# Kernel optimization log

Measured on AMD Instinct MI355X. Metric: run time of the kernel, lower is better.

Reference implementation:

```python
import jax, jax.numpy as jnp
import numpy as np

N, DF, DR, H, K = 4096, 128, 64, 1024, 10


def _init_linear(key, fan_in, fan_out):
    kw, kb = jax.random.split(key)
    bound = 1.0 / np.sqrt(fan_in)
    W = jax.random.uniform(kw, (fan_in, fan_out), jnp.float32, -bound, bound)
    b = jax.random.uniform(kb, (fan_out,), jnp.float32, -bound, bound)
    return W, b


def setup_inputs() -> dict:
    key = jax.random.key(0)
    ks = jax.random.split(key, 8)
    condition = jax.random.normal(ks[0], (N, DF), jnp.float32)
    tensor = jax.random.normal(ks[1], (N, DR), jnp.float32)
    Win, b_in = _init_linear(ks[2], DF + DR, H)
    W1, b1 = _init_linear(ks[3], H, H)
    W2, b2 = _init_linear(ks[4], H, H)
    W3, b3 = _init_linear(ks[5], H, H)
    Wout, b_out = _init_linear(ks[6], H, DR)
    return {"condition": condition, "tensor": tensor,
            "Win": Win, "b_in": b_in, "W1": W1, "b1": b1,
            "W2": W2, "b2": b2, "W3": W3, "b3": b3,
            "Wout": Wout, "b_out": b_out}


def _mlp(x, Win, b_in, W1, b1, W2, b2, W3, b3, Wout, b_out):
    # FFNN: input layer + 3 hidden layers with Softplus, linear output -> DR
    h = jax.nn.softplus(x @ Win + b_in)
    h = jax.nn.softplus(h @ W1 + b1)
    h = jax.nn.softplus(h @ W2 + b2)
    h = jax.nn.softplus(h @ W3 + b3)
    return h @ Wout + b_out


def reference(condition, tensor, Win, b_in, W1, b1, W2, b2, W3, b3, Wout, b_out):
    # torch.cdist(condition, condition), p=2 -> [N, N]
    sq = jnp.sum(condition * condition, axis=-1)
    d2 = sq[:, None] + sq[None, :] - 2.0 * (condition @ condition.T)
    dist = jnp.sqrt(jnp.maximum(d2, 0.0))
    # torch.topk(dist, 10, dim=1, largest=False) -> k nearest neighbor indices
    _, neighbor_idx = jax.lax.top_k(-dist, K)  # [N, K]
    # gather neighbor groups
    cond_g = condition[neighbor_idx]  # [N, K, DF]
    tens_g = tensor[neighbor_idx]     # [N, K, DR]
    # MongeMapNetwork.pushforward: tensor - MLP(concat(condition, tensor))
    x = jnp.concatenate([cond_g, tens_g], axis=-1)  # [N, K, DF+DR]
    pushed = tens_g - _mlp(x, Win, b_in, W1, b1, W2, b2, W3, b3, Wout, b_out)
    return pushed  # [N, K, DR]
```

## Files before the change

kernel.cpp:

```cpp
#include <hip/hip_runtime.h>
#include <hip/hip_fp16.h>
#include <stdint.h>

typedef unsigned short u16;
typedef unsigned int   u32;
typedef unsigned long long u64;
typedef short v8bf __attribute__((ext_vector_type(8)));
typedef float v4f  __attribute__((ext_vector_type(4)));
typedef u16   v8u  __attribute__((ext_vector_type(8)));

#define NPTS 4096
#define DF   128
#define DR   64
#define HID  1024
#define KNN  10
#define DIN  192

#define AS1 __attribute__((address_space(1)))
#define AS3 __attribute__((address_space(3)))

__device__ __forceinline__ float bf2f(u16 b){ return __uint_as_float(((unsigned)b)<<16); }
__device__ __forceinline__ u16 f2bf(float f){
  unsigned u = __float_as_uint(f);
  unsigned r = 0x7fffu + ((u>>16)&1u);
  return (u16)((u + r)>>16);
}
__device__ __forceinline__ u16 f2h(float f){
  __half h = __float2half(f);
  return __half_as_ushort(h);
}
__device__ __forceinline__ float softplus_f(float x){
  return x>15.f ? x : __logf(1.f + __expf(x));
}
__device__ __forceinline__ float rdv(const void* p, long j, int fl){
  return fl ? bf2f(((const u16*)p)[j]) : ((const float*)p)[j];
}
__device__ __forceinline__ void gl2lds16(const u16* g, u16* l){
  __builtin_amdgcn_global_load_lds((const AS1 unsigned int*)g, (AS3 unsigned int*)l, 16, 0, 0);
}

__global__ void detect_k(const u16* __restrict__ c, int* __restrict__ flag){
  __shared__ int cnt[256];
  int t = threadIdx.x, n = 0;
  for(int i=t; i<8192; i+=256){
    u16 v = c[2*i];
    int e = (v>>7)&0xff;
    n += (e>=96 && e<=158);
  }
  cnt[t] = n; __syncthreads();
  for(int s=128; s>0; s>>=1){ if(t<s) cnt[t]+=cnt[t+s]; __syncthreads(); }
  if(t==0) *flag = (cnt[0] > 4915) ? 1 : 0;
}

__global__ void prep_k(const void* cond, const void* tens,
    const void* Wi, const void* W1, const void* W2, const void* W3, const void* Wo,
    const void* bi, const void* b1, const void* b2, const void* b3, const void* bo,
    float* __restrict__ condF, float* __restrict__ tensF, float* __restrict__ biasF,
    u16* Oi, u16* O1, u16* O2, u16* O3, u16* Oo,
    float* __restrict__ sq, u16* __restrict__ X, const int* __restrict__ flag){
  __shared__ u16 tile[32][33];
  const int fl = *flag;
  const int bid = blockIdx.x, tid = threadIdx.x;
  if(bid < 3089){
    int i = bid*256 + tid;
    if(i < 524288){ condF[i] = rdv(cond, i, fl); }
    else if(i < 786432){ tensF[i-524288] = rdv(tens, i-524288, fl); }
    else{
      int j = i - 786432;
      if(j < 1024)      biasF[j] = rdv(bi, j, fl);
      else if(j < 2048) biasF[j] = rdv(b1, j-1024, fl);
      else if(j < 3072) biasF[j] = rdv(b2, j-2048, fl);
      else if(j < 4096) biasF[j] = rdv(b3, j-3072, fl);
      else if(j < 4160) biasF[j] = rdv(bo, j-4096, fl);
    }
  } else if(bid < 6417){
    int b = bid - 3089;
    const void* in; u16* out; int R, C, bx, by;
    if(b < 192)      {              in=Wi; out=Oi; R=192;  C=1024; bx=b&31; by=b>>5; }
    else if(b < 1216){ b -= 192;    in=W1; out=O1; R=1024; C=1024; bx=b&31; by=b>>5; }
    else if(b < 2240){ b -= 1216;   in=W2; out=O2; R=1024; C=1024; bx=b&31; by=b>>5; }
    else if(b < 3264){ b -= 2240;   in=W3; out=O3; R=1024; C=1024; bx=b&31; by=b>>5; }
    else             { b -= 3264;   in=Wo; out=Oo; R=1024; C=64;   bx=b&1;  by=b>>1; }
    int gx = bx*32, gy = by*32;
    int tx = tid&31, ty = tid>>5;
    #pragma unroll
    for(int r=ty; r<32; r+=8){
      size_t idx = (size_t)(gy+r)*C + gx + tx;
      tile[r][tx] = fl ? ((const u16*)in)[idx] : f2bf(((const float*)in)[idx]);
    }
    __syncthreads();
    #pragma unroll
    for(int r=ty; r<32; r+=8) out[(size_t)(gx+r)*R + gy + tx] = tile[tx][r];
  } else if(bid < 7441){
    int b = bid - 6417;
    int row = b*4 + (tid>>6), lane = tid&63;
    float a = rdv(cond, (long)row*DF + lane, fl);
    float c2 = rdv(cond, (long)row*DF + lane + 64, fl);
    double s = (double)a*a + (double)c2*c2;
    #pragma unroll
    for(int off=32; off>0; off>>=1) s += __shfl_down(s, off, 64);
    if(lane==0) sq[row] = (float)s;
  } else {
    int c = (bid-7441)*256 + tid;
    int j = c/48;
    int off = (c - j*48)*4;
    ushort4 o;
    if(off < DF){
      o.x = f2bf(rdv(cond, (long)j*DF + off + 0, fl));
      o.y = f2bf(rdv(cond, (long)j*DF + off + 1, fl));
      o.z = f2bf(rdv(cond, (long)j*DF + off + 2, fl));
      o.w = f2bf(rdv(cond, (long)j*DF + off + 3, fl));
    }else{
      int t2 = off - DF;
      o.x = f2bf(rdv(tens, (long)j*DR + t2 + 0, fl));
      o.y = f2bf(rdv(tens, (long)j*DR + t2 + 1, fl));
      o.z = f2bf(rdv(tens, (long)j*DR + t2 + 2, fl));
      o.w = f2bf(rdv(tens, (long)j*DR + t2 + 3, fl));
    }
    *(ushort4*)&X[(size_t)j*DIN + off] = o;
  }
}

__device__ __forceinline__ void gemm_bt_body(const u16* __restrict__ A,
    const u16* __restrict__ Bt, const float* __restrict__ bias, u16* __restrict__ C,
    int Nc, int Kc, int bid, u16* As, u16* Bs){
  const int xcd = bid&7, slot = bid>>3;
  const int bm = (xcd*4 + (slot>>4)) * 128;
  const int bn = (slot&15) * 64;
  const int tid = threadIdx.x, lane = tid&63, wave = tid>>6;
  const int wm = (wave&1)*64, wn = (wave>>1)*32;
  int c0 = wave*128 + lane, c1 = c0 + 64;
  int r0 = c0>>2, q0 = c0&3, r1 = c1>>2, q1 = c1&3;
  int cb = wave*64 + lane, rb = cb>>2, qb = cb&3;
  const u16* pA0 = A  + (size_t)(bm+r0)*Kc + q0*8;
  const u16* pA1 = A  + (size_t)(bm+r1)*Kc + q1*8;
  const u16* pB  = Bt + (size_t)(bn+rb)*Kc + qb*8;
  u16* lA0 = &As[wave*1024];
  u16* lA1 = &As[wave*1024 + 512];
  u16* lB  = &Bs[wave*512];
  const int m16 = lane&15, q = lane>>4;
  v4f acc[4][2] = {};
  for(int kb=0; kb<Kc; kb+=64){
    gl2lds16(pA0 + kb, lA0);
    gl2lds16(pA1 + kb, lA1);
    gl2lds16(pB  + kb, lB);
    gl2lds16(pA0 + kb + 32, lA0 + 4096);
    gl2lds16(pA1 + kb + 32, lA1 + 4096);
    gl2lds16(pB  + kb + 32, lB + 2048);
    __syncthreads();
    #pragma unroll
    for(int kk=0;kk<2;kk++){
      v8bf a[4], b[2];
      #pragma unroll
      for(int x=0;x<4;x++) a[x] = *(const v8bf*)&As[kk*4096 + (wm + x*16 + m16)*32 + q*8];
      #pragma unroll
      for(int x=0;x<2;x++) b[x] = *(const v8bf*)&Bs[kk*2048 + (wn + x*16 + m16)*32 + q*8];
      #pragma unroll
      for(int mi=0;mi<4;mi++)
        #pragma unroll
        for(int ni=0;ni<2;ni++)
          acc[mi][ni] = __builtin_amdgcn_mfma_f32_16x16x32_bf16(a[mi], b[ni], acc[mi][ni], 0,0,0);
    }
    __syncthreads();
  }
  const int col16 = lane&15, rowq = lane>>4;
  #pragma unroll
  for(int mi=0;mi<4;mi++){
    #pragma unroll
    for(int ni=0;ni<2;ni++){
      int cn = bn + wn + ni*16 + col16;
      float bi = bias[cn];
      #pragma unroll
      for(int r=0;r<4;r++){
        int rw = bm + wm + mi*16 + rowq*4 + r;
        float v = softplus_f(acc[mi][ni][r] + bi);
        C[(size_t)rw*Nc + cn] = f2bf(v);
      }
    }
  }
}

__device__ __forceinline__ void knn_body(const u16* __restrict__ distH,
    const float* __restrict__ condF, int* __restrict__ nidx, int row,
    float* __restrict__ af, int* __restrict__ scnt,
    int* __restrict__ cand, u64* __restrict__ keys){
  const int lane = threadIdx.x&63;
  af[lane]    = condF[(size_t)row*DF + lane];
  af[lane+64] = condF[(size_t)row*DF + lane + 64];
  if(lane==0) *scnt = 0;
  const v8u* drow = (const v8u*)(distH + (size_t)row*NPTS);
  v8u vals[8];
  #pragma unroll
  for(int k=0;k<8;k++) vals[k] = drow[lane + k*64];
  u32 mx = 0;
  #pragma unroll
  for(int k=0;k<8;k++)
    #pragma unroll
    for(int e=0;e<8;e++){ u32 v = vals[k][e]; mx = v>mx ? v : mx; }
  #pragma unroll
  for(int off=32; off>0; off>>=1){
    u32 o = (u32)__shfl_down((int)mx, off, 64); mx = o>mx ? o : mx;
  }
  mx = (u32)__shfl((int)mx, 0, 64);
  u32 hi = mx+1, lo = 0;
  for(int it=0; it<17; ++it){
    u32 mid = (lo+hi)>>1;
    int c = 0;
    #pragma unroll
    for(int k=0;k<8;k++)
      #pragma unroll
      for(int e=0;e<8;e++) c += ((u32)vals[k][e] < mid);
    #pragma unroll
    for(int off=32; off>0; off>>=1) c += __shfl_down(c, off, 64);
    c = __shfl(c, 0, 64);
    if(c >= 16){ hi = mid; if(c <= 48) break; }
    else lo = mid;
  }
  const u32 t = hi;
  #pragma unroll
  for(int k=0;k<8;k++)
    #pragma unroll
    for(int e=0;e<8;e++){
      if((u32)vals[k][e] < t){
        int s = atomicAdd(scnt, 1);
        if(s < 64) cand[s] = (lane + k*64)*8 + e;
      }
    }
  int cnt = *scnt; if(cnt > 64) cnt = 64;
  u64 mykey = ~0ULL; int myj = -1;
  if(lane < cnt){
    int j = cand[lane];
    const float4* bp4 = (const float4*)(condF + (size_t)j*DF);
    double s = 0.0;
    #pragma unroll
    for(int v4i=0; v4i<32; v4i++){
      float4 bv = bp4[v4i];
      double d0 = (double)af[v4i*4+0]-(double)bv.x;
      double d1 = (double)af[v4i*4+1]-(double)bv.y;
      double d2 = (double)af[v4i*4+2]-(double)bv.z;
      double d3 = (double)af[v4i*4+3]-(double)bv.w;
      s += d0*d0 + d1*d1 + d2*d2 + d3*d3;
    }
    u64 bits = (u64)__double_as_longlong(s);
    mykey = (bits & ~0xFFFULL) | (u32)j;
    myj = j;
  }
  keys[lane] = mykey;
  if(lane < cnt){
    int rank = 0;
    for(int c2=0;c2<cnt;c2++) rank += (keys[c2] < mykey);
    if(rank < KNN) nidx[row*KNN + rank] = myj;
  }
}

__global__ __launch_bounds__(256,2) void gram_g1_k(const u16* __restrict__ condB,
    const float* __restrict__ condF, const float* __restrict__ sq,
    u16* __restrict__ distH, const int* __restrict__ flag,
    const u16* __restrict__ X, const u16* __restrict__ Wt_in,
    const float* __restrict__ biasF, u16* __restrict__ A0){
  __shared__ __align__(16) u16 smem[20480];
  const int bid = blockIdx.x;
  if(bid < 512){
    gemm_bt_body(X, Wt_in, biasF, A0, HID, DIN, bid, smem, smem+8192);
    return;
  }
  const int gb = bid - 512;
  u16* Ahi = smem;
  u16* Alo = smem + 5120;
  u16* Bhi = smem + 10240;
  u16* Blo = smem + 15360;
  const int fl = *flag;
  const int bm = (gb&31)*128, bn = (gb>>5)*128;
  const int tid = threadIdx.x, lane = tid&63, wave = tid>>6;
  const int wm = (wave&1)*64, wn = (wave>>1)*64;
  v4f acc[4][4] = {};
  for(int kb=0; kb<DF; kb+=32){
    if(fl){
      #pragma unroll
      for(int t=0;t<2;t++){
        int c2 = tid + t*256;
        int r = c2>>2, col = (c2&3)*8;
        *(uint4*)&Ahi[r*40+col] = *(const uint4*)&condB[(size_t)(bm+r)*DF + kb + col];
        *(uint4*)&Bhi[r*40+col] = *(const uint4*)&condB[(size_t)(bn+r)*DF + kb + col];
      }
    }else{
      #pragma unroll
      for(int t=0;t<4;t++){
        int ch = tid + t*256;
        int r = ch>>3, c = (ch&7)*4;
        float4 av = *(const float4*)&condF[(size_t)(bm+r)*DF + kb + c];
        float4 bv = *(const float4*)&condF[(size_t)(bn+r)*DF + kb + c];
        ushort4 ah, bh, al, bl;
        ah.x=f2bf(av.x); ah.y=f2bf(av.y); ah.z=f2bf(av.z); ah.w=f2bf(av.w);
        bh.x=f2bf(bv.x); bh.y=f2bf(bv.y); bh.z=f2bf(bv.z); bh.w=f2bf(bv.w);
        al.x=f2bf(av.x-bf2f(ah.x)); al.y=f2bf(av.y-bf2f(ah.y));
        al.z=f2bf(av.z-bf2f(ah.z)); al.w=f2bf(av.w-bf2f(ah.w));
        bl.x=f2bf(bv.x-bf2f(bh.x)); bl.y=f2bf(bv.y-bf2f(bh.y));
        bl.z=f2bf(bv.z-bf2f(bh.z)); bl.w=f2bf(bv.w-bf2f(bh.w));
        *(ushort4*)&Ahi[r*40+c] = ah; *(ushort4*)&Bhi[r*40+c] = bh;
        *(ushort4*)&Alo[r*40+c] = al; *(ushort4*)&Blo[r*40+c] = bl;
      }
    }
    __syncthreads();
    const int m16 = lane&15, q = lane>>4;
    v8bf ahf[4], bhf[4];
    #pragma unroll
    for(int x=0;x<4;x++){
      ahf[x] = *(const v8bf*)&Ahi[(wm + x*16 + m16)*40 + q*8];
      bhf[x] = *(const v8bf*)&Bhi[(wn + x*16 + m16)*40 + q*8];
    }
    if(!fl){
      v8bf alf[4], blf[4];
      #pragma unroll
      for(int x=0;x<4;x++){
        alf[x] = *(const v8bf*)&Alo[(wm + x*16 + m16)*40 + q*8];
        blf[x] = *(const v8bf*)&Blo[(wn + x*16 + m16)*40 + q*8];
      }
      #pragma unroll
      for(int mi=0;mi<4;mi++)
        #pragma unroll
        for(int ni=0;ni<4;ni++){
          acc[mi][ni] = __builtin_amdgcn_mfma_f32_16x16x32_bf16(alf[mi], bhf[ni], acc[mi][ni], 0,0,0);
          acc[mi][ni] = __builtin_amdgcn_mfma_f32_16x16x32_bf16(ahf[mi], blf[ni], acc[mi][ni], 0,0,0);
        }
    }
    #pragma unroll
    for(int mi=0;mi<4;mi++)
      #pragma unroll
      for(int ni=0;ni<4;ni++)
        acc[mi][ni] = __builtin_amdgcn_mfma_f32_16x16x32_bf16(ahf[mi], bhf[ni], acc[mi][ni], 0,0,0);
    __syncthreads();
  }
  const int col16 = lane&15, rowq = lane>>4;
  #pragma unroll
  for(int mi=0;mi<4;mi++){
    #pragma unroll
    for(int ni=0;ni<4;ni++){
      int cj = bn + wn + ni*16 + col16;
      float sqj = sq[cj];
      #pragma unroll
      for(int r=0;r<4;r++){
        int ri = bm + wm + mi*16 + rowq*4 + r;
        float d2 = (sq[ri] + sqj) - 2.0f*acc[mi][ni][r];
        distH[(size_t)ri*NPTS + cj] = f2h(fmaxf(d2, 0.f));
      }
    }
  }
}

__global__ __launch_bounds__(256,2) void gemm_knn_k(const u16* __restrict__ A,
    const u16* __restrict__ Bt, const float* __restrict__ bias, u16* __restrict__ C,
    const u16* __restrict__ distH, const float* __restrict__ condF,
    int* __restrict__ nidx, int rowoff){
  __shared__ __align__(16) u16 gsm[12288];
  __shared__ float af[4][DF];
  __shared__ int   scnt[4];
  __shared__ int   cand[4][64];
  __shared__ u64   keys[4][64];
  const int bid = blockIdx.x;
  if(bid < 512){
    gemm_bt_body(A, Bt, bias, C, HID, HID, bid, gsm, gsm+8192);
  } else {
    const int wv = threadIdx.x>>6;
    const int row = rowoff + (bid-512)*4 + wv;
    knn_body(distH, condF, nidx, row, af[wv], &scnt[wv], cand[wv], keys[wv]);
  }
}

__global__ __launch_bounds__(256,2) void gemm_bt_k(const u16* __restrict__ A,
    const u16* __restrict__ Bt, const float* __restrict__ bias, u16* __restrict__ C){
  __shared__ __align__(16) u16 As[8192];
  __shared__ __align__(16) u16 Bs[4096];
  gemm_bt_body(A, Bt, bias, C, HID, HID, blockIdx.x, As, Bs);
}

__global__ __launch_bounds__(256,2) void gemm_out_k(const u16* __restrict__ A,
    const u16* __restrict__ Bt, float* __restrict__ Pp){
  __shared__ __align__(16) u16 As[128*32];
  __shared__ __align__(16) u16 Bs[64*32];
  const int bm = (blockIdx.x>>2)*128;
  const int k0 = (blockIdx.x&3)*256;
  float* P = Pp + (size_t)(blockIdx.x&3)*262144;
  const int tid = threadIdx.x, lane = tid&63, wave = tid>>6;
  const int wm = wave*32;
  int c0 = wave*128 + lane, c1 = c0 + 64;
  int ra0 = c0>>2, qa0 = c0&3, ra1 = c1>>2, qa1 = c1&3;
  int cb = wave*64 + lane;
  int rb = cb>>2, qb = cb&3;
  const u16* pA0 = A  + (size_t)(bm+ra0)*HID + qa0*8;
  const u16* pA1 = A  + (size_t)(bm+ra1)*HID + qa1*8;
  const u16* pB  = Bt + (size_t)rb*HID + qb*8;
  u16* lA0 = &As[(wave*128     )*8];
  u16* lA1 = &As[(wave*128 + 64)*8];
  u16* lB  = &Bs[(wave*64      )*8];
  const int m16 = lane&15, q = lane>>4;
  v4f acc[2][4] = {};
  for(int kb=k0; kb<k0+256; kb+=32){
    gl2lds16(pA0 + kb, lA0);
    gl2lds16(pA1 + kb, lA1);
    gl2lds16(pB  + kb, lB);
    __syncthreads();
    v8bf a[2], b[4];
    a[0] = *(const v8bf*)&As[(wm + m16)*32 + q*8];
    a[1] = *(const v8bf*)&As[(wm + 16 + m16)*32 + q*8];
    #pragma unroll
    for(int x=0;x<4;x++) b[x] = *(const v8bf*)&Bs[(x*16 + m16)*32 + q*8];
    #pragma unroll
    for(int mi=0;mi<2;mi++)
      #pragma unroll
      for(int ni=0;ni<4;ni++)
        acc[mi][ni] = __builtin_amdgcn_mfma_f32_16x16x32_bf16(a[mi], b[ni], acc[mi][ni], 0,0,0);
    __syncthreads();
  }
  const int col16 = lane&15, rowq = lane>>4;
  #pragma unroll
  for(int mi=0;mi<2;mi++){
    #pragma unroll
    for(int ni=0;ni<4;ni++){
      int cn = ni*16 + col16;
      #pragma unroll
      for(int r=0;r<4;r++){
        int rw = bm + wm + mi*16 + rowq*4 + r;
        P[(size_t)rw*DR + cn] = acc[mi][ni][r];
      }
    }
  }
}

__global__ void gather_k(const float* __restrict__ Pp, const float* __restrict__ tensF,
                         const float* __restrict__ biasF, const int* __restrict__ nidx,
                         void* __restrict__ outv, const int* __restrict__ flag){
  const int fl = *flag;
  int e = blockIdx.x*256 + threadIdx.x;
  int m = e>>4;
  int c = (e&15)*4;
  int j = nidx[m] & (NPTS-1);
  size_t rc = (size_t)j*DR + c;
  float4 t  = *(const float4*)&tensF[rc];
  float4 b  = *(const float4*)&biasF[4096 + c];
  float4 p0 = *(const float4*)&Pp[rc];
  float4 p1 = *(const float4*)&Pp[262144 + rc];
  float4 p2 = *(const float4*)&Pp[524288 + rc];
  float4 p3 = *(const float4*)&Pp[786432 + rc];
  float4 v;
  v.x = t.x - (b.x + ((p0.x+p1.x)+(p2.x+p3.x)));
  v.y = t.y - (b.y + ((p0.y+p1.y)+(p2.y+p3.y)));
  v.z = t.z - (b.z + ((p0.z+p1.z)+(p2.z+p3.z)));
  v.w = t.w - (b.w + ((p0.w+p1.w)+(p2.w+p3.w)));
  if(fl){
    ushort4 o; o.x=f2bf(v.x); o.y=f2bf(v.y); o.z=f2bf(v.z); o.w=f2bf(v.w);
    *(ushort4*)&((u16*)outv)[(size_t)m*DR + c] = o;
  }else{
    *(float4*)&((float*)outv)[(size_t)m*DR + c] = v;
  }
}

constexpr size_t OFF_FLAG  = 0;
constexpr size_t OFF_SQ    = 256;
constexpr size_t OFF_NIDX  = OFF_SQ    + 16384;
constexpr size_t OFF_BIAS  = OFF_NIDX  + 163840;
constexpr size_t OFF_CONDF = OFF_BIAS  + 16640;
constexpr size_t OFF_TENSF = OFF_CONDF + 2097152;
constexpr size_t OFF_WTIN  = OFF_TENSF + 1048576;
constexpr size_t OFF_WT1   = OFF_WTIN  + 393216;
constexpr size_t OFF_WT2   = OFF_WT1   + 2097152;
constexpr size_t OFF_WT3   = OFF_WT2   + 2097152;
constexpr size_t OFF_WTO   = OFF_WT3   + 2097152;
constexpr size_t OFF_DIST  = OFF_WTO   + 131072;
constexpr size_t OFF_X     = OFF_DIST  + 33554432;
constexpr size_t OFF_A0    = OFF_X     + 1572864;
constexpr size_t OFF_A1    = OFF_A0    + 8388608;
constexpr size_t OFF_P     = OFF_A1    + 8388608;

extern "C" void kernel_launch(void* const* d_in, const int* in_sizes, int n_in,
                              void* d_out, int out_size, void* d_ws, size_t ws_size,
                              hipStream_t stream){
  char* ws = (char*)d_ws;
  int*   flag  = (int*)  (ws + OFF_FLAG);
  float* sqv   = (float*)(ws + OFF_SQ);
  int*   nidx  = (int*)  (ws + OFF_NIDX);
  float* biasF = (float*)(ws + OFF_BIAS);
  float* condF = (float*)(ws + OFF_CONDF);
  float* tensF = (float*)(ws + OFF_TENSF);
  u16*   Wt_in = (u16*)  (ws + OFF_WTIN);
  u16*   Wt1   = (u16*)  (ws + OFF_WT1);
  u16*   Wt2   = (u16*)  (ws + OFF_WT2);
  u16*   Wt3   = (u16*)  (ws + OFF_WT3);
  u16*   Wt_o  = (u16*)  (ws + OFF_WTO);
  u16*   distH = (u16*)  (ws + OFF_DIST);
  u16*   X     = (u16*)  (ws + OFF_X);
  u16*   A0    = (u16*)  (ws + OFF_A0);
  u16*   A1    = (u16*)  (ws + OFF_A1);
  float* Pp    = (float*)(ws + OFF_P);

  detect_k <<<1, 256, 0, stream>>>((const u16*)d_in[0], flag);
  prep_k   <<<8209, 256, 0, stream>>>(d_in[0], d_in[1],
                d_in[2], d_in[4], d_in[6], d_in[8], d_in[10],
                d_in[3], d_in[5], d_in[7], d_in[9], d_in[11],
                condF, tensF, biasF, Wt_in, Wt1, Wt2, Wt3, Wt_o, sqv, X, flag);
  gram_g1_k<<<1536, 256, 0, stream>>>((const u16*)d_in[0], condF, sqv, distH, flag,
                                      X, Wt_in, biasF, A0);
  gemm_knn_k<<<1024, 256, 0, stream>>>(A0, Wt1, biasF+1024, A1, distH, condF, nidx, 0);
  gemm_knn_k<<<1024, 256, 0, stream>>>(A1, Wt2, biasF+2048, A0, distH, condF, nidx, 2048);
  gemm_bt_k  <<<512, 256, 0, stream>>>(A0, Wt3, biasF+3072, A1);
  gemm_out_k <<<128, 256, 0, stream>>>(A1, Wt_o, Pp);
  gather_k   <<<2560, 256, 0, stream>>>(Pp, tensF, biasF, nidx, d_out, flag);
}
```

Measured before the change: 209.6 us.

## Double-buffer LDS tiles in GEMM bodies to overlap global loads with MFMA

```diff
diff --git a/kernel.cpp b/kernel.cpp
--- a/kernel.cpp
+++ b/kernel.cpp
@@ -135,34 +135,42 @@
   const u16* pA0 = A  + (size_t)(bm+r0)*Kc + q0*8;
   const u16* pA1 = A  + (size_t)(bm+r1)*Kc + q1*8;
   const u16* pB  = Bt + (size_t)(bn+rb)*Kc + qb*8;
-  u16* lA0 = &As[wave*1024];
-  u16* lA1 = &As[wave*1024 + 512];
-  u16* lB  = &Bs[wave*512];
   const int m16 = lane&15, q = lane>>4;
   v4f acc[4][2] = {};
-  for(int kb=0; kb<Kc; kb+=64){
-    gl2lds16(pA0 + kb, lA0);
-    gl2lds16(pA1 + kb, lA1);
-    gl2lds16(pB  + kb, lB);
-    gl2lds16(pA0 + kb + 32, lA0 + 4096);
-    gl2lds16(pA1 + kb + 32, lA1 + 4096);
-    gl2lds16(pB  + kb + 32, lB + 2048);
+  const int NT = Kc>>6;
+
+#define STG_BT(kb, ao, bo) do{ \
+    gl2lds16(pA0 + (kb),      &As[(ao) + wave*1024]);        \
+    gl2lds16(pA1 + (kb),      &As[(ao) + wave*1024 + 512]);  \
+    gl2lds16(pB  + (kb),      &Bs[(bo) + wave*512]);         \
+    gl2lds16(pA0 + (kb) + 32, &As[(ao) + 4096 + wave*1024]);       \
+    gl2lds16(pA1 + (kb) + 32, &As[(ao) + 4096 + wave*1024 + 512]); \
+    gl2lds16(pB  + (kb) + 32, &Bs[(bo) + 2048 + wave*512]);  \
+  }while(0)
+
+  STG_BT(0, 0, 0);
+  int cur = 0;
+  for(int t=0; t<NT; ++t){
     __syncthreads();
+    if(t+1 < NT) STG_BT((t+1)<<6, (cur^1)*8192, (cur^1)*4096);
+    const u16* Ab = &As[cur*8192];
+    const u16* Bb = &Bs[cur*4096];
     #pragma unroll
     for(int kk=0;kk<2;kk++){
       v8bf a[4], b[2];
       #pragma unroll
-      for(int x=0;x<4;x++) a[x] = *(const v8bf*)&As[kk*4096 + (wm + x*16 + m16)*32 + q*8];
-      #pragma unroll
-      for(int x=0;x<2;x++) b[x] = *(const v8bf*)&Bs[kk*2048 + (wn + x*16 + m16)*32 + q*8];
+      for(int x=0;x<4;x++) a[x] = *(const v8bf*)&Ab[kk*4096 + (wm + x*16 + m16)*32 + q*8];
+      #pragma unroll
+      for(int x=0;x<2;x++) b[x] = *(const v8bf*)&Bb[kk*2048 + (wn + x*16 + m16)*32 + q*8];
       #pragma unroll
       for(int mi=0;mi<4;mi++)
         #pragma unroll
         for(int ni=0;ni<2;ni++)
           acc[mi][ni] = __builtin_amdgcn_mfma_f32_16x16x32_bf16(a[mi], b[ni], acc[mi][ni], 0,0,0);
     }
-    __syncthreads();
-  }
+    cur ^= 1;
+  }
+#undef STG_BT
   const int col16 = lane&15, rowq = lane>>4;
   #pragma unroll
   for(int mi=0;mi<4;mi++){
@@ -258,10 +266,10 @@
     u16* __restrict__ distH, const int* __restrict__ flag,
     const u16* __restrict__ X, const u16* __restrict__ Wt_in,
     const float* __restrict__ biasF, u16* __restrict__ A0){
-  __shared__ __align__(16) u16 smem[20480];
+  __shared__ __align__(16) u16 smem[24576];
   const int bid = blockIdx.x;
   if(bid < 512){
-    gemm_bt_body(X, Wt_in, biasF, A0, HID, DIN, bid, smem, smem+8192);
+    gemm_bt_body(X, Wt_in, biasF, A0, HID, DIN, bid, smem, smem+16384);
     return;
   }
   const int gb = bid - 512;
@@ -352,14 +360,14 @@
     const u16* __restrict__ Bt, const float* __restrict__ bias, u16* __restrict__ C,
     const u16* __restrict__ distH, const float* __restrict__ condF,
     int* __restrict__ nidx, int rowoff){
-  __shared__ __align__(16) u16 gsm[12288];
+  __shared__ __align__(16) u16 gsm[24576];
   __shared__ float af[4][DF];
   __shared__ int   scnt[4];
   __shared__ int   cand[4][64];
   __shared__ u64   keys[4][64];
   const int bid = blockIdx.x;
   if(bid < 512){
-    gemm_bt_body(A, Bt, bias, C, HID, HID, bid, gsm, gsm+8192);
+    gemm_bt_body(A, Bt, bias, C, HID, HID, bid, gsm, gsm+16384);
   } else {
     const int wv = threadIdx.x>>6;
     const int row = rowoff + (bid-512)*4 + wv;
@@ -369,15 +377,15 @@
 
 __global__ __launch_bounds__(256,2) void gemm_bt_k(const u16* __restrict__ A,
     const u16* __restrict__ Bt, const float* __restrict__ bias, u16* __restrict__ C){
-  __shared__ __align__(16) u16 As[8192];
-  __shared__ __align__(16) u16 Bs[4096];
+  __shared__ __align__(16) u16 As[16384];
+  __shared__ __align__(16) u16 Bs[8192];
   gemm_bt_body(A, Bt, bias, C, HID, HID, blockIdx.x, As, Bs);
 }
 
 __global__ __launch_bounds__(256,2) void gemm_out_k(const u16* __restrict__ A,
     const u16* __restrict__ Bt, float* __restrict__ Pp){
-  __shared__ __align__(16) u16 As[128*32];
-  __shared__ __align__(16) u16 Bs[64*32];
+  __shared__ __align__(16) u16 As[16384];
+  __shared__ __align__(16) u16 Bs[8192];
   const int bm = (blockIdx.x>>2)*128;
   const int k0 = (blockIdx.x&3)*256;
   float* P = Pp + (size_t)(blockIdx.x&3)*262144;
@@ -390,28 +398,41 @@
   const u16* pA0 = A  + (size_t)(bm+ra0)*HID + qa0*8;
   const u16* pA1 = A  + (size_t)(bm+ra1)*HID + qa1*8;
   const u16* pB  = Bt + (size_t)rb*HID + qb*8;
-  u16* lA0 = &As[(wave*128     )*8];
-  u16* lA1 = &As[(wave*128 + 64)*8];
-  u16* lB  = &Bs[(wave*64      )*8];
   const int m16 = lane&15, q = lane>>4;
   v4f acc[2][4] = {};
-  for(int kb=k0; kb<k0+256; kb+=32){
-    gl2lds16(pA0 + kb, lA0);
-    gl2lds16(pA1 + kb, lA1);
-    gl2lds16(pB  + kb, lB);
+
+#define STG_OUT(kb, ao, bo) do{ \
+    gl2lds16(pA0 + (kb),      &As[(ao) + wave*1024]);        \
+    gl2lds16(pA1 + (kb),      &As[(ao) + wave*1024 + 512]);  \
+    gl2lds16(pB  + (kb),      &Bs[(bo) + wave*512]);         \
+    gl2lds16(pA0 + (kb) + 32, &As[(ao) + 4096 + wave*1024]);       \
+    gl2lds16(pA1 + (kb) + 32, &As[(ao) + 4096 + wave*1024 + 512]); \
+    gl2lds16(pB  + (kb) + 32, &Bs[(bo) + 2048 + wave*512]);  \
+  }while(0)
+
+  STG_OUT(k0, 0, 0);
+  int cur = 0;
+  for(int t=0; t<4; ++t){
     __syncthreads();
-    v8bf a[2], b[4];
-    a[0] = *(const v8bf*)&As[(wm + m16)*32 + q*8];
-    a[1] = *(const v8bf*)&As[(wm + 16 + m16)*32 + q*8];
-    #pragma unroll
-    for(int x=0;x<4;x++) b[x] = *(const v8bf*)&Bs[(x*16 + m16)*32 + q*8];
-    #pragma unroll
-    for(int mi=0;mi<2;mi++)
-      #pragma unroll
-      for(int ni=0;ni<4;ni++)
-        acc[mi][ni] = __builtin_amdgcn_mfma_f32_16x16x32_bf16(a[mi], b[ni], acc[mi][ni], 0,0,0);
-    __syncthreads();
-  }
+    if(t+1 < 4) STG_OUT(k0 + ((t+1)<<6), (cur^1)*8192, (cur^1)*4096);
+    const u16* Ab = &As[cur*8192];
+    const u16* Bb = &Bs[cur*4096];
+    #pragma unroll
+    for(int kk=0;kk<2;kk++){
+      v8bf a[2], b[4];
+      a[0] = *(const v8bf*)&Ab[kk*4096 + (wm + m16)*32 + q*8];
+      a[1] = *(const v8bf*)&Ab[kk*4096 + (wm + 16 + m16)*32 + q*8];
+      #pragma unroll
+      for(int x=0;x<4;x++) b[x] = *(const v8bf*)&Bb[kk*2048 + (x*16 + m16)*32 + q*8];
+      #pragma unroll
+      for(int mi=0;mi<2;mi++)
+        #pragma unroll
+        for(int ni=0;ni<4;ni++)
+          acc[mi][ni] = __builtin_amdgcn_mfma_f32_16x16x32_bf16(a[mi], b[ni], acc[mi][ni], 0,0,0);
+    }
+    cur ^= 1;
+  }
+#undef STG_OUT
   const int col16 = lane&15, rowq = lane>>4;
   #pragma unroll
   for(int mi=0;mi<2;mi++){
```

Measured after the change: 217.8 us. 3.9% more time.

## Triple-buffer LDS staging in GEMM bodies with vmcnt-based prefetch pipelining

Applied to the files above, without the earlier changes.

```diff
diff --git a/kernel.cpp b/kernel.cpp
--- a/kernel.cpp
+++ b/kernel.cpp
@@ -38,6 +38,10 @@
 __device__ __forceinline__ void gl2lds16(const u16* g, u16* l){
   __builtin_amdgcn_global_load_lds((const AS1 unsigned int*)g, (AS3 unsigned int*)l, 16, 0, 0);
 }
+#define WAITV12 asm volatile("s_waitcnt vmcnt(12)" ::: "memory")
+#define WAITV6  asm volatile("s_waitcnt vmcnt(6)"  ::: "memory")
+#define WAITV0  asm volatile("s_waitcnt vmcnt(0)"  ::: "memory")
+#define CFENCE  asm volatile("" ::: "memory")
 
 __global__ void detect_k(const u16* __restrict__ c, int* __restrict__ flag){
   __shared__ int cnt[256];
@@ -135,34 +139,54 @@
   const u16* pA0 = A  + (size_t)(bm+r0)*Kc + q0*8;
   const u16* pA1 = A  + (size_t)(bm+r1)*Kc + q1*8;
   const u16* pB  = Bt + (size_t)(bn+rb)*Kc + qb*8;
-  u16* lA0 = &As[wave*1024];
-  u16* lA1 = &As[wave*1024 + 512];
-  u16* lB  = &Bs[wave*512];
   const int m16 = lane&15, q = lane>>4;
   v4f acc[4][2] = {};
-  for(int kb=0; kb<Kc; kb+=64){
-    gl2lds16(pA0 + kb, lA0);
-    gl2lds16(pA1 + kb, lA1);
-    gl2lds16(pB  + kb, lB);
-    gl2lds16(pA0 + kb + 32, lA0 + 4096);
-    gl2lds16(pA1 + kb + 32, lA1 + 4096);
-    gl2lds16(pB  + kb + 32, lB + 2048);
-    __syncthreads();
-    #pragma unroll
-    for(int kk=0;kk<2;kk++){
-      v8bf a[4], b[2];
-      #pragma unroll
-      for(int x=0;x<4;x++) a[x] = *(const v8bf*)&As[kk*4096 + (wm + x*16 + m16)*32 + q*8];
-      #pragma unroll
-      for(int x=0;x<2;x++) b[x] = *(const v8bf*)&Bs[kk*2048 + (wn + x*16 + m16)*32 + q*8];
-      #pragma unroll
-      for(int mi=0;mi<4;mi++)
-        #pragma unroll
-        for(int ni=0;ni<2;ni++)
-          acc[mi][ni] = __builtin_amdgcn_mfma_f32_16x16x32_bf16(a[mi], b[ni], acc[mi][ni], 0,0,0);
-    }
-    __syncthreads();
-  }
+  const int NT = Kc>>6;
+
+#define STG_BT(t, buf) do{ int kb=(t)<<6; \
+    gl2lds16(pA0 + kb,      &As[(buf)*8192 + wave*1024]);        \
+    gl2lds16(pA1 + kb,      &As[(buf)*8192 + wave*1024 + 512]);  \
+    gl2lds16(pB  + kb,      &Bs[(buf)*4096 + wave*512]);         \
+    gl2lds16(pA0 + kb + 32, &As[(buf)*8192 + 4096 + wave*1024]);       \
+    gl2lds16(pA1 + kb + 32, &As[(buf)*8192 + 4096 + wave*1024 + 512]); \
+    gl2lds16(pB  + kb + 32, &Bs[(buf)*4096 + 2048 + wave*512]);  \
+  }while(0)
+#define CMP_BT(buf) do{ \
+    const u16* Ab = &As[(buf)*8192]; \
+    const u16* Bb = &Bs[(buf)*4096]; \
+    _Pragma("unroll") \
+    for(int kk=0;kk<2;kk++){ \
+      v8bf a[4], b[2]; \
+      _Pragma("unroll") \
+      for(int x=0;x<4;x++) a[x] = *(const v8bf*)&Ab[kk*4096 + (wm + x*16 + m16)*32 + q*8]; \
+      _Pragma("unroll") \
+      for(int x=0;x<2;x++) b[x] = *(const v8bf*)&Bb[kk*2048 + (wn + x*16 + m16)*32 + q*8]; \
+      _Pragma("unroll") \
+      for(int mi=0;mi<4;mi++) \
+        _Pragma("unroll") \
+        for(int ni=0;ni<2;ni++) \
+          acc[mi][ni] = __builtin_amdgcn_mfma_f32_16x16x32_bf16(a[mi], b[ni], acc[mi][ni], 0,0,0); \
+    } \
+  }while(0)
+
+  STG_BT(0, 0); STG_BT(1, 1); STG_BT(2, 2);
+  int t = 0, cur = 0;
+  for(; t < NT-3; ++t){
+    WAITV12;
+    __builtin_amdgcn_s_barrier(); CFENCE;
+    CMP_BT(cur);
+    CFENCE; __builtin_amdgcn_s_barrier(); CFENCE;
+    STG_BT(t+3, cur);
+    cur = cur==2 ? 0 : cur+1;
+  }
+  WAITV12; __builtin_amdgcn_s_barrier(); CFENCE;
+  CMP_BT(cur); cur = cur==2 ? 0 : cur+1;
+  WAITV6;  __builtin_amdgcn_s_barrier(); CFENCE;
+  CMP_BT(cur); cur = cur==2 ? 0 : cur+1;
+  WAITV0;  __builtin_amdgcn_s_barrier(); CFENCE;
+  CMP_BT(cur);
+#undef STG_BT
+#undef CMP_BT
   const int col16 = lane&15, rowq = lane>>4;
   #pragma unroll
   for(int mi=0;mi<4;mi++){
@@ -258,10 +282,10 @@
     u16* __restrict__ distH, const int* __restrict__ flag,
     const u16* __restrict__ X, const u16* __restrict__ Wt_in,
     const float* __restrict__ biasF, u16* __restrict__ A0){
-  __shared__ __align__(16) u16 smem[20480];
+  __shared__ __align__(16) u16 smem[36864];
   const int bid = blockIdx.x;
   if(bid < 512){
-    gemm_bt_body(X, Wt_in, biasF, A0, HID, DIN, bid, smem, smem+8192);
+    gemm_bt_body(X, Wt_in, biasF, A0, HID, DIN, bid, smem, smem+24576);
     return;
   }
   const int gb = bid - 512;
@@ -352,14 +376,14 @@
     const u16* __restrict__ Bt, const float* __restrict__ bias, u16* __restrict__ C,
     const u16* __restrict__ distH, const float* __restrict__ condF,
     int* __restrict__ nidx, int rowoff){
-  __shared__ __align__(16) u16 gsm[12288];
+  __shared__ __align__(16) u16 gsm[36864];
   __shared__ float af[4][DF];
   __shared__ int   scnt[4];
   __shared__ int   cand[4][64];
   __shared__ u64   keys[4][64];
   const int bid = blockIdx.x;
   if(bid < 512){
-    gemm_bt_body(A, Bt, bias, C, HID, HID, bid, gsm, gsm+8192);
+    gemm_bt_body(A, Bt, bias, C, HID, HID, bid, gsm, gsm+24576);
   } else {
     const int wv = threadIdx.x>>6;
     const int row = rowoff + (bid-512)*4 + wv;
@@ -369,15 +393,15 @@
 
 __global__ __launch_bounds__(256,2) void gemm_bt_k(const u16* __restrict__ A,
     const u16* __restrict__ Bt, const float* __restrict__ bias, u16* __restrict__ C){
-  __shared__ __align__(16) u16 As[8192];
-  __shared__ __align__(16) u16 Bs[4096];
+  __shared__ __align__(16) u16 As[24576];
+  __shared__ __align__(16) u16 Bs[12288];
   gemm_bt_body(A, Bt, bias, C, HID, HID, blockIdx.x, As, Bs);
 }
 
 __global__ __launch_bounds__(256,2) void gemm_out_k(const u16* __restrict__ A,
     const u16* __restrict__ Bt, float* __restrict__ Pp){
-  __shared__ __align__(16) u16 As[128*32];
-  __shared__ __align__(16) u16 Bs[64*32];
+  __shared__ __align__(16) u16 As[24576];
+  __shared__ __align__(16) u16 Bs[12288];
   const int bm = (blockIdx.x>>2)*128;
   const int k0 = (blockIdx.x&3)*256;
   float* P = Pp + (size_t)(blockIdx.x&3)*262144;
@@ -390,28 +414,48 @@
   const u16* pA0 = A  + (size_t)(bm+ra0)*HID + qa0*8;
   const u16* pA1 = A  + (size_t)(bm+ra1)*HID + qa1*8;
   const u16* pB  = Bt + (size_t)rb*HID + qb*8;
-  u16* lA0 = &As[(wave*128     )*8];
-  u16* lA1 = &As[(wave*128 + 64)*8];
-  u16* lB  = &Bs[(wave*64      )*8];
   const int m16 = lane&15, q = lane>>4;
   v4f acc[2][4] = {};
-  for(int kb=k0; kb<k0+256; kb+=32){
-    gl2lds16(pA0 + kb, lA0);
-    gl2lds16(pA1 + kb, lA1);
-    gl2lds16(pB  + kb, lB);
-    __syncthreads();
-    v8bf a[2], b[4];
-    a[0] = *(const v8bf*)&As[(wm + m16)*32 + q*8];
-    a[1] = *(const v8bf*)&As[(wm + 16 + m16)*32 + q*8];
-    #pragma unroll
-    for(int x=0;x<4;x++) b[x] = *(const v8bf*)&Bs[(x*16 + m16)*32 + q*8];
-    #pragma unroll
-    for(int mi=0;mi<2;mi++)
-      #pragma unroll
-      for(int ni=0;ni<4;ni++)
-        acc[mi][ni] = __builtin_amdgcn_mfma_f32_16x16x32_bf16(a[mi], b[ni], acc[mi][ni], 0,0,0);
-    __syncthreads();
-  }
+
+#define STG_OUT(t, buf) do{ int kb = k0 + ((t)<<6); \
+    gl2lds16(pA0 + kb,      &As[(buf)*8192 + wave*1024]);        \
+    gl2lds16(pA1 + kb,      &As[(buf)*8192 + wave*1024 + 512]);  \
+    gl2lds16(pB  + kb,      &Bs[(buf)*4096 + wave*512]);         \
+    gl2lds16(pA0 + kb + 32, &As[(buf)*8192 + 4096 + wave*1024]);       \
+    gl2lds16(pA1 + kb + 32, &As[(buf)*8192 + 4096 + wave*1024 + 512]); \
+    gl2lds16(pB  + kb + 32, &Bs[(buf)*4096 + 2048 + wave*512]);  \
+  }while(0)
+#define CMP_OUT(buf) do{ \
+    const u16* Ab = &As[(buf)*8192]; \
+    const u16* Bb = &Bs[(buf)*4096]; \
+    _Pragma("unroll") \
+    for(int kk=0;kk<2;kk++){ \
+      v8bf a[2], b[4]; \
+      a[0] = *(const v8bf*)&Ab[kk*4096 + (wm + m16)*32 + q*8]; \
+      a[1] = *(const v8bf*)&Ab[kk*4096 + (wm + 16 + m16)*32 + q*8]; \
+      _Pragma("unroll") \
+      for(int x=0;x<4;x++) b[x] = *(const v8bf*)&Bb[kk*2048 + (x*16 + m16)*32 + q*8]; \
+      _Pragma("unroll") \
+      for(int mi=0;mi<2;mi++) \
+        _Pragma("unroll") \
+        for(int ni=0;ni<4;ni++) \
+          acc[mi][ni] = __builtin_amdgcn_mfma_f32_16x16x32_bf16(a[mi], b[ni], acc[mi][ni], 0,0,0); \
+    } \
+  }while(0)
+
+  STG_OUT(0,0); STG_OUT(1,1); STG_OUT(2,2);
+  WAITV12; __builtin_amdgcn_s_barrier(); CFENCE;
+  CMP_OUT(0);
+  CFENCE; __builtin_amdgcn_s_barrier(); CFENCE;
+  STG_OUT(3, 0);
+  WAITV12; __builtin_amdgcn_s_barrier(); CFENCE;
+  CMP_OUT(1);
+  WAITV6;  __builtin_amdgcn_s_barrier(); CFENCE;
+  CMP_OUT(2);
+  WAITV0;  __builtin_amdgcn_s_barrier(); CFENCE;
+  CMP_OUT(0);
+#undef STG_OUT
+#undef CMP_OUT
   const int col16 = lane&15, rowq = lane>>4;
   #pragma unroll
   for(int mi=0;mi<2;mi++){
```

New measurement: 219.8 us. +4.9%, slower.
